# Performance work log

Measured on AMD Instinct MI355X. Metric: run time of the kernel, lower is better.

Reference implementation:

```python
import jax, jax.numpy as jnp
import numpy as np

N_HEADS = 12
HEAD_DIM = 64
HIDDEN = 768


def _split_heads(t):
    # [B, S, H*D] -> [B, H, S, D]
    b, s, _ = t.shape
    return t.reshape(b, s, N_HEADS, HEAD_DIM).transpose(0, 2, 1, 3)


def setup_inputs() -> dict:
    key = jax.random.key(0)
    B, S = 4, 2048
    x = jax.random.normal(key, (B, S, 3 * HIDDEN), dtype=jnp.float32)
    # GPT-2 causal bias buffer: lower-triangular True = attend
    causal_mask = jnp.tril(jnp.ones((S, S), dtype=bool))[None, None, :, :]
    return {"input": x, "causal_mask": causal_mask}


def reference(input, causal_mask):
    query, key, value = jnp.split(input, 3, axis=2)  # each [B, S, 768]
    q = _split_heads(query)   # [B, H, S, D]
    k = _split_heads(key)
    v = _split_heads(value)
    scale = jnp.asarray(HEAD_DIM ** 0.5, dtype=q.dtype)
    attn_weights = jnp.einsum('bhqd,bhkd->bhqk', q, k) / scale
    mask_value = jnp.finfo(attn_weights.dtype).min
    attn_weights = jnp.where(causal_mask, attn_weights, mask_value)
    attn_weights = jax.nn.softmax(attn_weights, axis=-1).astype(v.dtype)
    # attn_dropout(p=0.1) is identity in eval mode; omitted for determinism
    attn_output = jnp.einsum('bhqk,bhkd->bhqd', attn_weights, v)
    return (attn_output, attn_weights)
```

## Files before the change

### kernel.cpp

```cpp
#include <hip/hip_runtime.h>
#include <hip/hip_bf16.h>


#define S_LEN 2048
#define DH    64
#define NHD   12
#define H3    2304
#define QT    64
#define KTILE 64
#define NT    32
#define PSTR  72
#define VSTR  72
#define KBUFE (KTILE * DH)
#define VBUFE (DH * VSTR)
#define OSZ   (4 * NHD * S_LEN * DH)
#define SCALE2 0.18033688011112042f

typedef __attribute__((ext_vector_type(8))) short short8;
typedef __attribute__((ext_vector_type(4))) short short4e;
typedef __attribute__((ext_vector_type(4))) float f32x4;

__device__ __forceinline__ short bfc(float x) {
  return (short)__builtin_bit_cast(unsigned short, __float2bfloat16(x));
}
__device__ __forceinline__ float b2f(unsigned short u) {
  return __builtin_bit_cast(float, (unsigned int)u << 16);
}
__device__ __forceinline__ short8 pack8(const float4 a, const float4 b) {
  short8 r;
  r[0] = bfc(a.x); r[1] = bfc(a.y); r[2] = bfc(a.z); r[3] = bfc(a.w);
  r[4] = bfc(b.x); r[5] = bfc(b.y); r[6] = bfc(b.z); r[7] = bfc(b.w);
  return r;
}

template <int F32>
__global__ __launch_bounds__(256, 3)
void attn_fused(const void* __restrict__ xv, void* __restrict__ ov)
{
  __shared__ __align__(16) unsigned short k_lds[2 * KBUFE];
  __shared__ __align__(16) unsigned short v_lds[2 * VBUFE];
  __shared__ __align__(16) unsigned short p_lds[QT * PSTR];

  const int tid  = threadIdx.x;
  const int wave = tid >> 6;
  const int lane = tid & 63;
  const int quad = lane >> 4;
  const int l16  = lane & 15;

  const unsigned int* xw = (const unsigned int*)xv;
  int cnt = 0;
  #pragma unroll
  for (int j = 0; j < 32; ++j) {
    const unsigned e = (xw[j] >> 7) & 0xFFu;
    cnt += (e >= 100u && e <= 150u) ? 1 : 0;
  }
  const bool isf32 = (cnt < 24);
  if (isf32 != (bool)F32) return;

  const unsigned short* xh = (const unsigned short*)xv;
  const float*          xf = (const float*)xv;

  const int qb = (NT - 1) - blockIdx.x;
  const int bh = blockIdx.y;
  const int b  = bh / NHD;
  const int h  = bh - b * NHD;
  const int q_base = qb * QT;

  const int qrow = q_base + wave * 16 + l16;
  const size_t qoff = (size_t)(b * S_LEN + qrow) * H3 + h * DH + quad * 8;
  short8 qa0, qa1;
  if constexpr (F32) {
    qa0 = pack8(*(const float4*)(xf + qoff),      *(const float4*)(xf + qoff + 4));
    qa1 = pack8(*(const float4*)(xf + qoff + 32), *(const float4*)(xf + qoff + 36));
  } else {
    qa0 = *(const short8*)(xh + qoff);
    qa1 = *(const short8*)(xh + qoff + 32);
  }

  const int sl   = tid & 7;
  const int row0 = tid >> 3;
  const int ksl  = (sl ^ (row0 & 7)) << 3;
  const int kwo0 = row0 * DH + ksl;
  const int kwo1 = (row0 + 32) * DH + ksl;
  const int vk0  = row0 ^ (sl << 3);
  const int vk1  = (row0 + 32) ^ (sl << 3);
  const size_t koff0 = ((size_t)b * S_LEN + row0) * H3 + 768 + h * DH + sl * 8;
  const size_t koff1 = ((size_t)b * S_LEN + row0 + 32) * H3 + 768 + h * DH + sl * 8;

  const int qg0 = q_base + wave * 16 + quad * 4;

  float4 fK[4]; short8 hK[2];
  float4 fV[4]; short8 hV[2];

  auto issueK = [&](int kt) {
    const size_t t = (size_t)kt * KTILE * H3;
    if constexpr (F32) {
      fK[0] = *(const float4*)(xf + koff0 + t);
      fK[1] = *(const float4*)(xf + koff0 + t + 4);
      fK[2] = *(const float4*)(xf + koff1 + t);
      fK[3] = *(const float4*)(xf + koff1 + t + 4);
    } else {
      hK[0] = *(const short8*)(xh + koff0 + t);
      hK[1] = *(const short8*)(xh + koff1 + t);
    }
  };
  auto issueV = [&](int kt) {
    const size_t t = (size_t)kt * KTILE * H3 + 768;
    if constexpr (F32) {
      fV[0] = *(const float4*)(xf + koff0 + t);
      fV[1] = *(const float4*)(xf + koff0 + t + 4);
      fV[2] = *(const float4*)(xf + koff1 + t);
      fV[3] = *(const float4*)(xf + koff1 + t + 4);
    } else {
      hV[0] = *(const short8*)(xh + koff0 + t);
      hV[1] = *(const short8*)(xh + koff1 + t);
    }
  };
  auto writeK = [&](int bb) {
    short8 s0, s1;
    if constexpr (F32) { s0 = pack8(fK[0], fK[1]); s1 = pack8(fK[2], fK[3]); }
    else               { s0 = hK[0];               s1 = hK[1]; }
    unsigned short* kb = k_lds + bb * KBUFE;
    *(short8*)&kb[kwo0] = s0;
    *(short8*)&kb[kwo1] = s1;
  };
  auto writeV = [&](int bb) {
    short8 v0, v1;
    if constexpr (F32) { v0 = pack8(fV[0], fV[1]); v1 = pack8(fV[2], fV[3]); }
    else               { v0 = hV[0];               v1 = hV[1]; }
    unsigned short* vb = v_lds + bb * VBUFE;
    #pragma unroll
    for (int j = 0; j < 8; ++j) {
      vb[(sl * 8 + j) * VSTR + vk0] = (unsigned short)v0[j];
      vb[(sl * 8 + j) * VSTR + vk1] = (unsigned short)v1[j];
    }
  };

  auto compute_scores = [&](int kbuf, int kt, bool diag, float (&sc)[4][4]) {
    const unsigned short* kbase = k_lds + kbuf * KBUFE;
    #pragma unroll
    for (int n16 = 0; n16 < 4; ++n16) {
      const unsigned short* krow = kbase + (n16 * 16 + l16) * DH;
      const short8 kb0 = *(const short8*)(krow + (((quad    ) ^ (l16 & 7)) << 3));
      const short8 kb1 = *(const short8*)(krow + (((quad + 4) ^ (l16 & 7)) << 3));
      f32x4 acc = {0.f, 0.f, 0.f, 0.f};
      __builtin_amdgcn_s_setprio(1);
      acc = __builtin_amdgcn_mfma_f32_16x16x32_bf16(qa0, kb0, acc, 0, 0, 0);
      acc = __builtin_amdgcn_mfma_f32_16x16x32_bf16(qa1, kb1, acc, 0, 0, 0);
      __builtin_amdgcn_s_setprio(0);
      if (diag) {
        const int keyg = kt * KTILE + n16 * 16 + l16;
        #pragma unroll
        for (int r = 0; r < 4; ++r)
          sc[n16][r] = (keyg <= qg0 + r) ? acc[r] * SCALE2 : -1e30f;
      } else {
        #pragma unroll
        for (int r = 0; r < 4; ++r)
          sc[n16][r] = acc[r] * SCALE2;
      }
    }
  };

  float l_part[4] = {0.f, 0.f, 0.f, 0.f};

  issueK(0);
  writeK(0);
  if (qb >= 1) issueK(1);
  __syncthreads();

  for (int kt = 0; kt <= qb; ++kt) {
    if (kt < qb)     writeK((kt + 1) & 1);
    if (kt + 1 < qb) issueK(kt + 2);

    float sc[4][4];
    compute_scores(kt & 1, kt, kt == qb, sc);

    #pragma unroll
    for (int r = 0; r < 4; ++r) {
      l_part[r] += (__builtin_amdgcn_exp2f(sc[0][r]) + __builtin_amdgcn_exp2f(sc[1][r]))
                 + (__builtin_amdgcn_exp2f(sc[2][r]) + __builtin_amdgcn_exp2f(sc[3][r]));
    }
    __syncthreads();
  }

  float b_r[4];
  #pragma unroll
  for (int r = 0; r < 4; ++r) {
    float s = l_part[r];
    #pragma unroll
    for (int sh = 1; sh < 16; sh <<= 1) s += __shfl_xor(s, sh, 64);
    b_r[r] = -__log2f(s);
  }

  f32x4 o_acc[4];
  #pragma unroll
  for (int m16 = 0; m16 < 4; ++m16) o_acc[m16] = (f32x4){0.f, 0.f, 0.f, 0.f};

  const size_t wbase = ((size_t)bh * S_LEN + q_base + wave * 16) * S_LEN;
  float*          wrF = (float*)ov + OSZ + wbase;
  unsigned short* wrH = (unsigned short*)ov + OSZ + wbase;

  issueK(0); issueV(0);
  writeK(0); writeV(0);
  if (qb >= 1) { issueK(1); issueV(1); }
  __syncthreads();

  for (int kt = 0; kt <= qb; ++kt) {
    if (kt < qb)     { writeK((kt + 1) & 1); writeV((kt + 1) & 1); }
    if (kt + 1 < qb) { issueK(kt + 2); issueV(kt + 2); }

    float sc[4][4];
    compute_scores(kt & 1, kt, kt == qb, sc);

    #pragma unroll
    for (int n16 = 0; n16 < 4; ++n16) {
      #pragma unroll
      for (int r = 0; r < 4; ++r) {
        const float p = __builtin_amdgcn_exp2f(sc[n16][r] + b_r[r]);
        p_lds[(wave * 16 + quad * 4 + r) * PSTR + n16 * 16 + l16] =
            (unsigned short)bfc(p);
      }
    }
    asm volatile("s_waitcnt lgkmcnt(0)" ::: "memory");

    const unsigned short* pr = &p_lds[(wave * 16 + l16) * PSTR + quad * 8];
    const short8 pb0 = *(const short8*)pr;
    const short8 pb1 = *(const short8*)(pr + 32);

    const unsigned short* vbase = v_lds + (kt & 1) * VBUFE;
    #pragma unroll
    for (int m16 = 0; m16 < 4; ++m16) {
      const int sd = ((m16 << 1) + (l16 >> 3)) & 7;
      const unsigned short* vrow = vbase + (m16 * 16 + l16) * VSTR;
      const short8 va0 = *(const short8*)(vrow + ((quad ^ sd) << 3));
      const short8 va1 = *(const short8*)(vrow + (((quad + 4) ^ sd) << 3));
      __builtin_amdgcn_s_setprio(1);
      o_acc[m16] = __builtin_amdgcn_mfma_f32_16x16x32_bf16(va0, pb0, o_acc[m16], 0, 0, 0);
      o_acc[m16] = __builtin_amdgcn_mfma_f32_16x16x32_bf16(va1, pb1, o_acc[m16], 0, 0, 0);
      __builtin_amdgcn_s_setprio(0);
    }

    #pragma unroll
    for (int i = 0; i < 2; ++i) {
      const int c = lane + i * 64;
      const int row = c >> 3, col8 = c & 7;
      const short8 pw = *(const short8*)&p_lds[(wave * 16 + row) * PSTR + col8 * 8];
      if (F32) {
        float* d = wrF + (size_t)row * S_LEN + kt * KTILE + col8 * 8;
        f32x4 w0 = {b2f(pw[0]), b2f(pw[1]), b2f(pw[2]), b2f(pw[3])};
        f32x4 w1 = {b2f(pw[4]), b2f(pw[5]), b2f(pw[6]), b2f(pw[7])};
        __builtin_nontemporal_store(w0, (f32x4*)d);
        __builtin_nontemporal_store(w1, (f32x4*)(d + 4));
      } else {
        __builtin_nontemporal_store(
            pw, (short8*)&wrH[(size_t)row * S_LEN + kt * KTILE + col8 * 8]);
      }
    }
    __syncthreads();
  }

  const f32x4 z4 = {0.f, 0.f, 0.f, 0.f};
  const short8 z8 = {0, 0, 0, 0, 0, 0, 0, 0};
  for (int kt = qb + 1; kt < NT; ++kt) {
    #pragma unroll
    for (int i = 0; i < 2; ++i) {
      const int c = lane + i * 64;
      const int row = c >> 3, col8 = c & 7;
      if (F32) {
        float* d = wrF + (size_t)row * S_LEN + kt * KTILE + col8 * 8;
        __builtin_nontemporal_store(z4, (f32x4*)d);
        __builtin_nontemporal_store(z4, (f32x4*)(d + 4));
      } else {
        __builtin_nontemporal_store(
            z8, (short8*)&wrH[(size_t)row * S_LEN + kt * KTILE + col8 * 8]);
      }
    }
  }

  const size_t obase = ((size_t)bh * S_LEN + q_base + wave * 16 + l16) * DH;
  #pragma unroll
  for (int m16 = 0; m16 < 4; ++m16) {
    const int d = m16 * 16 + quad * 4;
    if (F32) {
      __builtin_nontemporal_store(o_acc[m16], (f32x4*)&((float*)ov)[obase + d]);
    } else {
      short4e o;
      #pragma unroll
      for (int r = 0; r < 4; ++r) o[r] = bfc(o_acc[m16][r]);
      __builtin_nontemporal_store(o, (short4e*)&((unsigned short*)ov)[obase + d]);
    }
  }
}

extern "C" void kernel_launch(void* const* d_in, const int* in_sizes, int n_in,
                              void* d_out, int out_size, void* d_ws, size_t ws_size,
                              hipStream_t stream) {
  dim3 grid(NT, 4 * NHD);
  attn_fused<1><<<grid, 256, 0, stream>>>(d_in[0], d_out);
  attn_fused<0><<<grid, 256, 0, stream>>>(d_in[0], d_out);
}
```

Before: 1.031 ms.

## Double query tile to 128 rows with 512-thread blocks and remap block order

Each block now processes 128 query rows using 8 waves of 512 threads, so every K/V tile loaded into shared memory serves twice as many queries. Each thread loads a single K/V row segment per tile. Causal masking is now applied per wave based on its minimum query row rather than only on the final tile. Block indices are permuted so that consecutive blocks spread across heads and query tiles, balancing load across XCDs and CUs. The costs are coarser blocks with fewer of them, more imbalance within a block where some waves do masked-out work on the diagonal tiles, and heavier synchronization with 8 waves.

```diff
diff --git a/kernel.cpp b/kernel.cpp
--- a/kernel.cpp
+++ b/kernel.cpp
@@ -6,9 +6,11 @@
 #define DH    64
 #define NHD   12
 #define H3    2304
-#define QT    64
+#define QT    128
+#define NQT   16
 #define KTILE 64
 #define NT    32
+#define NBLK  (NQT * 4 * NHD)
 #define PSTR  72
 #define VSTR  72
 #define KBUFE (KTILE * DH)
@@ -34,7 +36,7 @@
 }
 
 template <int F32>
-__global__ __launch_bounds__(256, 3)
+__global__ __launch_bounds__(512, 4)
 void attn_fused(const void* __restrict__ xv, void* __restrict__ ov)
 {
   __shared__ __align__(16) unsigned short k_lds[2 * KBUFE];
@@ -60,11 +62,14 @@
   const unsigned short* xh = (const unsigned short*)xv;
   const float*          xf = (const float*)xv;
 
-  const int qb = (NT - 1) - blockIdx.x;
-  const int bh = blockIdx.y;
-  const int b  = bh / NHD;
-  const int h  = bh - b * NHD;
+  const int old = blockIdx.y * NQT + blockIdx.x;
+  const int nid = (old & 7) * (NBLK / 8) + (old >> 3);
+  const int qb  = (NQT - 1) - (nid & (NQT - 1));
+  const int bh  = nid >> 4;
+  const int b   = bh / NHD;
+  const int h   = bh - b * NHD;
   const int q_base = qb * QT;
+  const int NTL = 2 * qb + 2;
 
   const int qrow = q_base + wave * 16 + l16;
   const size_t qoff = (size_t)(b * S_LEN + qrow) * H3 + h * DH + quad * 8;
@@ -77,66 +82,52 @@
     qa1 = *(const short8*)(xh + qoff + 32);
   }
 
-  const int sl   = tid & 7;
-  const int row0 = tid >> 3;
-  const int ksl  = (sl ^ (row0 & 7)) << 3;
-  const int kwo0 = row0 * DH + ksl;
-  const int kwo1 = (row0 + 32) * DH + ksl;
-  const int vk0  = row0 ^ (sl << 3);
-  const int vk1  = (row0 + 32) ^ (sl << 3);
-  const size_t koff0 = ((size_t)b * S_LEN + row0) * H3 + 768 + h * DH + sl * 8;
-  const size_t koff1 = ((size_t)b * S_LEN + row0 + 32) * H3 + 768 + h * DH + sl * 8;
-
-  const int qg0 = q_base + wave * 16 + quad * 4;
-
-  float4 fK[4]; short8 hK[2];
-  float4 fV[4]; short8 hV[2];
+  const int sl  = tid & 7;
+  const int row = tid >> 3;
+  const int kwo = row * DH + ((sl ^ (row & 7)) << 3);
+  const int vk  = row ^ (sl << 3);
+  const size_t koff = ((size_t)b * S_LEN + row) * H3 + 768 + h * DH + sl * 8;
+
+  const int qg0  = q_base + wave * 16 + quad * 4;
+  const int qmin = q_base + wave * 16;
+
+  float4 fK[2]; short8 hK;
+  float4 fV[2]; short8 hV;
 
   auto issueK = [&](int kt) {
     const size_t t = (size_t)kt * KTILE * H3;
     if constexpr (F32) {
-      fK[0] = *(const float4*)(xf + koff0 + t);
-      fK[1] = *(const float4*)(xf + koff0 + t + 4);
-      fK[2] = *(const float4*)(xf + koff1 + t);
-      fK[3] = *(const float4*)(xf + koff1 + t + 4);
+      fK[0] = *(const float4*)(xf + koff + t);
+      fK[1] = *(const float4*)(xf + koff + t + 4);
     } else {
-      hK[0] = *(const short8*)(xh + koff0 + t);
-      hK[1] = *(const short8*)(xh + koff1 + t);
+      hK = *(const short8*)(xh + koff + t);
     }
   };
   auto issueV = [&](int kt) {
     const size_t t = (size_t)kt * KTILE * H3 + 768;
     if constexpr (F32) {
-      fV[0] = *(const float4*)(xf + koff0 + t);
-      fV[1] = *(const float4*)(xf + koff0 + t + 4);
-      fV[2] = *(const float4*)(xf + koff1 + t);
-      fV[3] = *(const float4*)(xf + koff1 + t + 4);
+      fV[0] = *(const float4*)(xf + koff + t);
+      fV[1] = *(const float4*)(xf + koff + t + 4);
     } else {
-      hV[0] = *(const short8*)(xh + koff0 + t);
-      hV[1] = *(const short8*)(xh + koff1 + t);
+      hV = *(const short8*)(xh + koff + t);
     }
   };
   auto writeK = [&](int bb) {
-    short8 s0, s1;
-    if constexpr (F32) { s0 = pack8(fK[0], fK[1]); s1 = pack8(fK[2], fK[3]); }
-    else               { s0 = hK[0];               s1 = hK[1]; }
-    unsigned short* kb = k_lds + bb * KBUFE;
-    *(short8*)&kb[kwo0] = s0;
-    *(short8*)&kb[kwo1] = s1;
+    short8 s;
+    if constexpr (F32) s = pack8(fK[0], fK[1]); else s = hK;
+    *(short8*)&k_lds[bb * KBUFE + kwo] = s;
   };
   auto writeV = [&](int bb) {
-    short8 v0, v1;
-    if constexpr (F32) { v0 = pack8(fV[0], fV[1]); v1 = pack8(fV[2], fV[3]); }
-    else               { v0 = hV[0];               v1 = hV[1]; }
+    short8 v;
+    if constexpr (F32) v = pack8(fV[0], fV[1]); else v = hV;
     unsigned short* vb = v_lds + bb * VBUFE;
     #pragma unroll
-    for (int j = 0; j < 8; ++j) {
-      vb[(sl * 8 + j) * VSTR + vk0] = (unsigned short)v0[j];
-      vb[(sl * 8 + j) * VSTR + vk1] = (unsigned short)v1[j];
-    }
-  };
-
-  auto compute_scores = [&](int kbuf, int kt, bool diag, float (&sc)[4][4]) {
+    for (int j = 0; j < 8; ++j)
+      vb[(sl * 8 + j) * VSTR + vk] = (unsigned short)v[j];
+  };
+
+  auto compute_scores = [&](int kbuf, int kt, float (&sc)[4][4]) {
+    const bool diag = (kt * KTILE + KTILE - 1) > qmin;
     const unsigned short* kbase = k_lds + kbuf * KBUFE;
     #pragma unroll
     for (int n16 = 0; n16 < 4; ++n16) {
@@ -165,15 +156,15 @@
 
   issueK(0);
   writeK(0);
-  if (qb >= 1) issueK(1);
+  if (NTL > 1) issueK(1);
   __syncthreads();
 
-  for (int kt = 0; kt <= qb; ++kt) {
-    if (kt < qb)     writeK((kt + 1) & 1);
-    if (kt + 1 < qb) issueK(kt + 2);
+  for (int kt = 0; kt < NTL; ++kt) {
+    if (kt + 1 < NTL) writeK((kt + 1) & 1);
+    if (kt + 2 < NTL) issueK(kt + 2);
 
     float sc[4][4];
-    compute_scores(kt & 1, kt, kt == qb, sc);
+    compute_scores(kt & 1, kt, sc);
 
     #pragma unroll
     for (int r = 0; r < 4; ++r) {
@@ -202,15 +193,15 @@
 
   issueK(0); issueV(0);
   writeK(0); writeV(0);
-  if (qb >= 1) { issueK(1); issueV(1); }
+  if (NTL > 1) { issueK(1); issueV(1); }
   __syncthreads();
 
-  for (int kt = 0; kt <= qb; ++kt) {
-    if (kt < qb)     { writeK((kt + 1) & 1); writeV((kt + 1) & 1); }
-    if (kt + 1 < qb) { issueK(kt + 2); issueV(kt + 2); }
+  for (int kt = 0; kt < NTL; ++kt) {
+    if (kt + 1 < NTL) { writeK((kt + 1) & 1); writeV((kt + 1) & 1); }
+    if (kt + 2 < NTL) { issueK(kt + 2); issueV(kt + 2); }
 
     float sc[4][4];
-    compute_scores(kt & 1, kt, kt == qb, sc);
+    compute_scores(kt & 1, kt, sc);
 
     #pragma unroll
     for (int n16 = 0; n16 < 4; ++n16) {
@@ -243,17 +234,17 @@
     #pragma unroll
     for (int i = 0; i < 2; ++i) {
       const int c = lane + i * 64;
-      const int row = c >> 3, col8 = c & 7;
-      const short8 pw = *(const short8*)&p_lds[(wave * 16 + row) * PSTR + col8 * 8];
+      const int prow = c >> 3, col8 = c & 7;
+      const short8 pw = *(const short8*)&p_lds[(wave * 16 + prow) * PSTR + col8 * 8];
       if (F32) {
-        float* d = wrF + (size_t)row * S_LEN + kt * KTILE + col8 * 8;
+        float* d = wrF + (size_t)prow * S_LEN + kt * KTILE + col8 * 8;
         f32x4 w0 = {b2f(pw[0]), b2f(pw[1]), b2f(pw[2]), b2f(pw[3])};
         f32x4 w1 = {b2f(pw[4]), b2f(pw[5]), b2f(pw[6]), b2f(pw[7])};
         __builtin_nontemporal_store(w0, (f32x4*)d);
         __builtin_nontemporal_store(w1, (f32x4*)(d + 4));
       } else {
         __builtin_nontemporal_store(
-            pw, (short8*)&wrH[(size_t)row * S_LEN + kt * KTILE + col8 * 8]);
+            pw, (short8*)&wrH[(size_t)prow * S_LEN + kt * KTILE + col8 * 8]);
       }
     }
     __syncthreads();
@@ -261,18 +252,18 @@
 
   const f32x4 z4 = {0.f, 0.f, 0.f, 0.f};
   const short8 z8 = {0, 0, 0, 0, 0, 0, 0, 0};
-  for (int kt = qb + 1; kt < NT; ++kt) {
+  for (int kt = NTL; kt < NT; ++kt) {
     #pragma unroll
     for (int i = 0; i < 2; ++i) {
       const int c = lane + i * 64;
-      const int row = c >> 3, col8 = c & 7;
+      const int prow = c >> 3, col8 = c & 7;
       if (F32) {
-        float* d = wrF + (size_t)row * S_LEN + kt * KTILE + col8 * 8;
+        float* d = wrF + (size_t)prow * S_LEN + kt * KTILE + col8 * 8;
         __builtin_nontemporal_store(z4, (f32x4*)d);
         __builtin_nontemporal_store(z4, (f32x4*)(d + 4));
       } else {
         __builtin_nontemporal_store(
-            z8, (short8*)&wrH[(size_t)row * S_LEN + kt * KTILE + col8 * 8]);
+            z8, (short8*)&wrH[(size_t)prow * S_LEN + kt * KTILE + col8 * 8]);
       }
     }
   }
@@ -295,7 +286,7 @@
 extern "C" void kernel_launch(void* const* d_in, const int* in_sizes, int n_in,
                               void* d_out, int out_size, void* d_ws, size_t ws_size,
                               hipStream_t stream) {
-  dim3 grid(NT, 4 * NHD);
-  attn_fused<1><<<grid, 256, 0, stream>>>(d_in[0], d_out);
-  attn_fused<0><<<grid, 256, 0, stream>>>(d_in[0], d_out);
-}
+  dim3 grid(NQT, 4 * NHD);
+  attn_fused<1><<<grid, 512, 0, stream>>>(d_in[0], d_out);
+  attn_fused<0><<<grid, 512, 0, stream>>>(d_in[0], d_out);
+}
```

New measurement: 1.085 ms. +5.3%, slower.
